# Kernel optimization log

Hardware: AMD Instinct MI355X
Metric: run time of the kernel (lower is better)

The kernel has to match this reference:

```python
import jax, jax.numpy as jnp
import numpy as np

# ---- model hyperparams (from init_kwargs) ----
N_USERS = 200000
N_ITEMS = 100000
DIM = 64
NNZ = 3000000
BATCH = 4096
N_HOPS = 3          # context_hops
EPS = 0.1           # SimGCL perturbation magnitude
TEMP = 0.2          # tau
CL_RATE = 0.5       # lamb
DECAY = 1e-4        # l2


def setup_inputs() -> dict:
    key = jax.random.key(0)
    k = jax.random.split(key, 8)
    user_embed = (jax.random.normal(k[0], (N_USERS, DIM), dtype=jnp.float32) * 0.01)
    item_embed = (jax.random.normal(k[1], (N_ITEMS, DIM), dtype=jnp.float32) * 0.01)
    N = N_USERS + N_ITEMS
    # COO normalized adjacency (buffer, not a parameter in the torch module)
    adj_rows = jax.random.randint(k[2], (NNZ,), 0, N)
    adj_cols = jax.random.randint(k[3], (NNZ,), 0, N)
    adj_vals = jax.random.uniform(k[4], (NNZ,), dtype=jnp.float32) * 0.2
    # unique index batches (torch code calls torch.unique for the CL loss;
    # sampling without replacement makes skipping unique exact, since the
    # InfoNCE mean is permutation invariant)
    users = jax.random.permutation(k[5], N_USERS)[:BATCH].astype(jnp.int32)
    pos_items = jax.random.permutation(k[6], N_ITEMS)[:BATCH].astype(jnp.int32)
    neg_items = jax.random.randint(k[7], (BATCH,), 0, N_ITEMS)
    return {"user_embed": user_embed, "item_embed": item_embed,
            "adj_vals": adj_vals, "adj_rows": adj_rows, "adj_cols": adj_cols,
            "users": users, "pos_items": pos_items, "neg_items": neg_items}


def _spmm(vals, rows, cols, x):
    # torch.sparse.mm(A, x) with A in COO form: out[r] += v * x[c]
    return jax.ops.segment_sum(vals[:, None] * x[cols], rows, num_segments=x.shape[0])


def _gcn(user_embed, item_embed, vals, rows, cols, perturbed, key):
    ego = jnp.concatenate([user_embed, item_embed], axis=0)  # [N, D]
    acc = jnp.zeros_like(ego)
    for h in range(N_HOPS):
        ego = _spmm(vals, rows, cols, ego)
        if perturbed:
            noise = jax.random.uniform(jax.random.fold_in(key, h), ego.shape, dtype=ego.dtype)
            noise = noise / jnp.maximum(jnp.linalg.norm(noise, axis=-1, keepdims=True), 1e-12)
            ego = ego + jnp.sign(ego) * noise * EPS
        acc = acc + ego
    mean = acc / N_HOPS   # stack + mean over hops == running-sum / n_hops
    return mean[:N_USERS], mean[N_USERS:]


def _info_nce(v1, v2, temp):
    v1 = v1 / jnp.maximum(jnp.linalg.norm(v1, axis=1, keepdims=True), 1e-12)
    v2 = v2 / jnp.maximum(jnp.linalg.norm(v2, axis=1, keepdims=True), 1e-12)
    pos = jnp.exp(jnp.sum(v1 * v2, axis=-1) / temp)              # [B]
    ttl = jnp.sum(jnp.exp((v1 @ v2.T) / temp), axis=1)           # [B]
    return jnp.mean(-jnp.log(pos / ttl + 1e-5))


def reference(user_embed, item_embed, adj_vals, adj_rows, adj_cols, users, pos_items, neg_items):
    # --- recommendation branch (no perturbation) ---
    ru, ri = _gcn(user_embed, item_embed, adj_vals, adj_rows, adj_cols, False, jax.random.key(0))
    ue, pe, ne = ru[users], ri[pos_items], ri[neg_items]
    pos_score = jnp.sum(ue * pe, axis=1)
    neg_score = jnp.sum(ue * ne, axis=1)
    rec_loss = jnp.mean(-jnp.log(1e-5 + jax.nn.sigmoid(pos_score - neg_score)))
    reg_loss = DECAY * (jnp.linalg.norm(ue) + jnp.linalg.norm(pe))  # Frobenius norms
    # --- contrastive branch: two perturbed views of the whole GCN ---
    u1, i1 = _gcn(user_embed, item_embed, adj_vals, adj_rows, adj_cols, True, jax.random.key(101))
    u2, i2 = _gcn(user_embed, item_embed, adj_vals, adj_rows, adj_cols, True, jax.random.key(202))
    cl_loss = CL_RATE * (_info_nce(u1[users], u2[users], TEMP)
                         + _info_nce(i1[pos_items], i2[pos_items], TEMP))
    return rec_loss + reg_loss + cl_loss
```

## Files before the change

kernel.cpp:

```cpp
#include <hip/hip_runtime.h>
#include <stdint.h>

#define NUSERS  200000
#define NITEMS  100000
#define NTOT    300000
#define DIM     64
#define NU64    (NUSERS * DIM)
#define NNZC    3000000
#define BATCH   4096
#define B64     (BATCH * DIM)
#define EPSP    0.1f
#define INV_TEMP 5.0f
#define SCAN_ELEMS 1024
#define GELEMS ((size_t)7 * B64 + 2 * BATCH + 8)

#define BSHIFT 11
#define BROWS  (1 << BSHIFT)
#define NB     ((NTOT + BROWS - 1) / BROWS)
#define CHUNK  4096
#define NCHUNK ((NNZC + CHUNK - 1) / CHUNK)
#define NH     (NB * NCHUNK)
#define CASTB  ((NTOT * DIM) / 2048)

typedef short bf16x8 __attribute__((ext_vector_type(8)));
typedef float f32x4  __attribute__((ext_vector_type(4)));

__device__ __forceinline__ float b2f(unsigned short h) {
  return __uint_as_float(((uint32_t)h) << 16);
}
__device__ __forceinline__ unsigned short f2b(float f) {
  uint32_t b = __float_as_uint(f);
  uint32_t r = b + 0x7FFFu + ((b >> 16) & 1u);
  return (unsigned short)(r >> 16);
}

__device__ __forceinline__ uint32_t mix32(uint32_t h) {
  h ^= h >> 16; h *= 0x85EBCA6Bu;
  h ^= h >> 13; h *= 0xC2B2AE35u;
  h ^= h >> 16;
  return h;
}
__device__ __forceinline__ uint32_t noise_key(uint32_t seed, uint32_t hop) {
  return mix32(seed * 0x9E3779B9u + hop * 0x85EBCA6Bu + 0x1BD11BDAu);
}
__device__ __forceinline__ float fast_unif(uint32_t key, uint32_t e) {
  uint32_t h = mix32(key + e * 0x9E3779B9u);
  return __uint_as_float((h >> 9) | 0x3F800000u) - 1.0f;
}
__device__ __forceinline__ float n_ss4(uint32_t key, uint32_t rq, float4& u) {
  uint32_t h = mix32(key + rq * 0x9E3779B9u);
  u.x = ((float)(h & 255u)         + 0.5f) * (1.0f / 256.0f);
  u.y = ((float)((h >> 8) & 255u)  + 0.5f) * (1.0f / 256.0f);
  u.z = ((float)((h >> 16) & 255u) + 0.5f) * (1.0f / 256.0f);
  u.w = ((float)(h >> 24)          + 0.5f) * (1.0f / 256.0f);
  return u.x * u.x + u.y * u.y + u.z * u.z + u.w * u.w;
}

__device__ __forceinline__ float sgnf(float a) {
  return (a > 0.f) ? 1.f : ((a < 0.f) ? -1.f : 0.f);
}

__global__ __launch_bounds__(256) void partA_cast(
    const int* __restrict__ rows, int* __restrict__ Hcnt,
    const float* __restrict__ uemb, const float* __restrict__ iemb,
    unsigned short* __restrict__ X0) {
  int blk = blockIdx.x;
  if (blk >= NCHUNK) {
    int base = (blk - NCHUNK) * 2048 + threadIdx.x * 8;
    const float* src = (base < NU64) ? (uemb + base) : (iemb + (base - NU64));
    float4 f0 = ((const float4*)src)[0];
    float4 f1 = ((const float4*)src)[1];
    uint4 o;
    o.x = ((uint32_t)f2b(f0.y) << 16) | f2b(f0.x);
    o.y = ((uint32_t)f2b(f0.w) << 16) | f2b(f0.z);
    o.z = ((uint32_t)f2b(f1.y) << 16) | f2b(f1.x);
    o.w = ((uint32_t)f2b(f1.w) << 16) | f2b(f1.z);
    *(uint4*)(X0 + base) = o;
    return;
  }
  __shared__ int bc[256];
  int c = blk, t = threadIdx.x;
  bc[t] = 0;
  __syncthreads();
  int base = c * CHUNK;
  for (int i = t; i < CHUNK; i += 256) {
    int e = base + i;
    if (e < NNZC) atomicAdd(&bc[rows[e] >> BSHIFT], 1);
  }
  __syncthreads();
  if (t < NB) Hcnt[t * NCHUNK + c] = bc[t];
}

__global__ void scan_block(const int* __restrict__ cnt, int* __restrict__ out,
                           int* __restrict__ bsums, int n) {
  __shared__ int tmp[SCAN_ELEMS];
  int base = blockIdx.x * SCAN_ELEMS;
  int t = threadIdx.x;
  #pragma unroll
  for (int q = 0; q < 4; ++q) {
    int k = t + q * 256, i = base + k;
    tmp[k] = (i < n) ? cnt[i] : 0;
  }
  __syncthreads();
  for (int off = 1; off < SCAN_ELEMS; off <<= 1) {
    int v[4];
    #pragma unroll
    for (int q = 0; q < 4; ++q) {
      int k = t + q * 256;
      v[q] = (k >= off) ? tmp[k - off] : 0;
    }
    __syncthreads();
    #pragma unroll
    for (int q = 0; q < 4; ++q) tmp[t + q * 256] += v[q];
    __syncthreads();
  }
  #pragma unroll
  for (int q = 0; q < 4; ++q) {
    int k = t + q * 256, i = base + k;
    if (i < n) out[i] = (k == 0) ? 0 : tmp[k - 1];
  }
  if (t == 0) bsums[blockIdx.x] = tmp[SCAN_ELEMS - 1];
}

__global__ void scan_sums(int* __restrict__ bsums, int nb) {
  __shared__ int tmp[512];
  int t = threadIdx.x;
  tmp[t] = (t < nb) ? bsums[t] : 0;
  __syncthreads();
  for (int off = 1; off < 512; off <<= 1) {
    int v = (t >= off) ? tmp[t - off] : 0;
    __syncthreads();
    tmp[t] += v;
    __syncthreads();
  }
  if (t < nb) bsums[t] = (t == 0) ? 0 : tmp[t - 1];
}

__global__ void add_offsets(int* __restrict__ out, const int* __restrict__ bsums,
                            int n) {
  int i = blockIdx.x * blockDim.x + threadIdx.x;
  if (i < n) out[i] += bsums[i / SCAN_ELEMS];
}

__global__ void add_offsets_emit(int* __restrict__ vmap,
                                 const int* __restrict__ bsums,
                                 const int* __restrict__ vflag,
                                 int* __restrict__ vlist,
                                 int* __restrict__ nV) {
  int i = blockIdx.x * blockDim.x + threadIdx.x;
  if (i >= NTOT) return;
  int m = vmap[i] + bsums[i / SCAN_ELEMS];
  vmap[i] = m;
  if (vflag[i]) vlist[m] = i;
  if (i == NTOT - 1) nV[0] = m + vflag[i];
}

__global__ __launch_bounds__(256) void partB(const float* __restrict__ vals,
                                             const int* __restrict__ rows,
                                             const int* __restrict__ cols,
                                             const int* __restrict__ Hofs,
                                             int2* __restrict__ midp,
                                             int* __restrict__ midr) {
  __shared__ int2 stv[CHUNK];
  __shared__ int  str_[CHUNK];
  __shared__ int  cnt[256];
  __shared__ int  sc[256];
  __shared__ int  adj[NB];
  int c = blockIdx.x, t = threadIdx.x;
  cnt[t] = 0;
  __syncthreads();
  int base = c * CHUNK;
  for (int i = t; i < CHUNK; i += 256) {
    int e = base + i;
    if (e < NNZC) atomicAdd(&cnt[rows[e] >> BSHIFT], 1);
  }
  __syncthreads();
  sc[t] = cnt[t];
  __syncthreads();
  for (int off = 1; off < 256; off <<= 1) {
    int u = (t >= off) ? sc[t - off] : 0;
    __syncthreads();
    sc[t] += u;
    __syncthreads();
  }
  int excl = sc[t] - cnt[t];
  cnt[t] = excl;
  if (t < NB) adj[t] = Hofs[t * NCHUNK + c] - excl;
  __syncthreads();
  for (int i = t; i < CHUNK; i += 256) {
    int e = base + i;
    if (e < NNZC) {
      int r = rows[e];
      int b = r >> BSHIFT;
      int p = atomicAdd(&cnt[b], 1);
      stv[p] = make_int2(__float_as_int(vals[e]), cols[e] * DIM);
      str_[p] = r;
    }
  }
  __syncthreads();
  int n = NNZC - base;
  if (n > CHUNK) n = CHUNK;
  for (int p = t; p < n; p += 256) {
    int r = str_[p];
    int b = r >> BSHIFT;
    int dst = adj[b] + p;
    midp[dst] = stv[p];
    midr[dst] = r;
  }
}

__global__ __launch_bounds__(256) void partC(const int2* __restrict__ midp,
                                             const int* __restrict__ midr,
                                             const int* __restrict__ Hofs,
                                             int* __restrict__ rs,
                                             int2* __restrict__ pairs) {
  __shared__ int h[BROWS];
  __shared__ int tsum[256];
  int b = blockIdx.x, t = threadIdx.x;
  int row0 = b << BSHIFT;
  for (int i = t; i < BROWS; i += 256) h[i] = 0;
  __syncthreads();
  int s = Hofs[b * NCHUNK];
  int e = (b + 1 < NB) ? Hofs[(b + 1) * NCHUNK] : NNZC;
  for (int p = s + t; p < e; p += 256)
    atomicAdd(&h[midr[p] - row0], 1);
  __syncthreads();
  int loc[8], run = 0;
  #pragma unroll
  for (int k = 0; k < 8; ++k) { loc[k] = run; run += h[t * 8 + k]; }
  tsum[t] = run;
  __syncthreads();
  for (int off = 1; off < 256; off <<= 1) {
    int v = (t >= off) ? tsum[t - off] : 0;
    __syncthreads();
    tsum[t] += v;
    __syncthreads();
  }
  int baseT = (t == 0) ? 0 : tsum[t - 1];
  #pragma unroll
  for (int k = 0; k < 8; ++k) {
    int i = t * 8 + k;
    int pos = s + baseT + loc[k];
    if (row0 + i < NTOT) rs[row0 + i] = pos;
    h[i] = pos;
  }
  if (b == NB - 1 && t == 0) rs[NTOT] = NNZC;
  __syncthreads();
  for (int p = s + t; p < e; p += 256) {
    int r = midr[p];
    int2 v = midp[p];
    int pos = atomicAdd(&h[r - row0], 1);
    pairs[pos] = v;
  }
}

__global__ __launch_bounds__(256) void mark_v(const int* __restrict__ u,
                                              const int* __restrict__ p,
                                              const int* __restrict__ n,
                                              const int* __restrict__ rs,
                                              const int2* __restrict__ pairs,
                                              int* __restrict__ vflag) {
  int i = blockIdx.x * 256 + threadIdx.x;
  if (i >= 3 * BATCH) return;
  int v = (i < BATCH) ? u[i]
        : (i < 2 * BATCH) ? (NUSERS + p[i - BATCH])
        : (NUSERS + n[i - 2 * BATCH]);
  vflag[v] = 1;
  int s = rs[v], e = rs[v + 1];
  for (int j = s; j < e; ++j) vflag[(unsigned)pairs[j].y >> 6] = 1;
}

template <bool PERT>
__global__ __launch_bounds__(256) void spmm_hop(
    const int2* __restrict__ pairs, const int* __restrict__ rs,
    const unsigned short* __restrict__ x,
    unsigned short* __restrict__ y, uint32_t seed, uint32_t hop) {
  int tid  = threadIdx.x;
  int lane = tid & 63;
  int q    = lane & 15;
  int wave = (blockIdx.x * 256 + tid) >> 6;
  int r    = wave * 4 + (lane >> 4);
  int s    = rs[r];
  int e    = rs[r + 1];
  int q4 = q * 4;
  float a0[4] = {0.f, 0.f, 0.f, 0.f};
  for (int j = s; j < e; j += 8) {
    int2 p[8];
    #pragma unroll
    for (int k = 0; k < 8; ++k)
      p[k] = (j + k < e) ? pairs[j + k] : make_int2(0, 0);
    #pragma unroll
    for (int k = 0; k < 8; ++k) {
      float v = __int_as_float(p[k].x);
      unsigned o = (unsigned)(p[k].y + q4);
      ushort4 h = *(const ushort4*)(x + o);
      a0[0] = fmaf(v, b2f(h.x), a0[0]); a0[1] = fmaf(v, b2f(h.y), a0[1]);
      a0[2] = fmaf(v, b2f(h.z), a0[2]); a0[3] = fmaf(v, b2f(h.w), a0[3]);
    }
  }
  int ebase = r * 64 + q4;
  if (PERT) {
    uint32_t key = noise_key(seed, hop);
    float u[4], ss = 0.f;
    #pragma unroll
    for (int k = 0; k < 4; ++k) {
      u[k] = fast_unif(key, (uint32_t)(ebase + k));
      ss += u[k] * u[k];
    }
    #pragma unroll
    for (int msk = 1; msk < 16; msk <<= 1) ss += __shfl_xor(ss, msk);
    float sc = EPSP / fmaxf(sqrtf(ss), 1e-12f);
    #pragma unroll
    for (int k = 0; k < 4; ++k) a0[k] += sgnf(a0[k]) * u[k] * sc;
  }
  ushort4 st;
  st.x = f2b(a0[0]); st.y = f2b(a0[1]); st.z = f2b(a0[2]); st.w = f2b(a0[3]);
  *(ushort4*)(y + ebase) = st;
}

__global__ __launch_bounds__(256) void spmm_sub3(
    const int2* __restrict__ pairs, const int* __restrict__ rs,
    const int* __restrict__ vlist, const int* __restrict__ nVp,
    const unsigned short* __restrict__ x,
    unsigned short* __restrict__ y0, unsigned short* __restrict__ y1,
    unsigned short* __restrict__ y2) {
  const uint32_t k101 = noise_key(101u, 0u);
  const uint32_t k202 = noise_key(202u, 0u);
  int nV = nVp[0];
  if (blockIdx.x * 16 >= nV) return;
  int tid  = threadIdx.x;
  int lane = tid & 63;
  int q    = lane & 15;
  int wave = (blockIdx.x * 256 + tid) >> 6;
  int slot = wave * 4 + (lane >> 4);
  if (slot >= nV) return;
  int v = vlist[slot];
  int s = rs[v];
  int e = rs[v + 1];
  int q4 = q * 4;
  float A0[4] = {0,0,0,0}, A1[4] = {0,0,0,0}, A2[4] = {0,0,0,0};
  for (int j = s; j < e; j += 8) {
    int2 p[8];
    #pragma unroll
    for (int k = 0; k < 8; ++k)
      p[k] = (j + k < e) ? pairs[j + k] : make_int2(0, 0);
    #pragma unroll
    for (int k = 0; k < 8; ++k) {
      float vv = __int_as_float(p[k].x);
      unsigned o = (unsigned)(p[k].y + q4);
      ushort4 h = *(const ushort4*)(x + o);
      float a[4] = {b2f(h.x), b2f(h.y), b2f(h.z), b2f(h.w)};
      float4 u1, u2;
      float s1 = n_ss4(k101, o >> 2, u1);
      float s2 = n_ss4(k202, o >> 2, u2);
      #pragma unroll
      for (int m = 1; m < 16; m <<= 1) {
        s1 += __shfl_xor(s1, m);
        s2 += __shfl_xor(s2, m);
      }
      float sc1 = EPSP / fmaxf(sqrtf(s1), 1e-12f);
      float sc2 = EPSP / fmaxf(sqrtf(s2), 1e-12f);
      float g0 = sgnf(a[0]), g1 = sgnf(a[1]), g2 = sgnf(a[2]), g3 = sgnf(a[3]);
      A0[0] = fmaf(vv, a[0], A0[0]); A0[1] = fmaf(vv, a[1], A0[1]);
      A0[2] = fmaf(vv, a[2], A0[2]); A0[3] = fmaf(vv, a[3], A0[3]);
      A1[0] = fmaf(vv, fmaf(g0 * u1.x, sc1, a[0]), A1[0]);
      A1[1] = fmaf(vv, fmaf(g1 * u1.y, sc1, a[1]), A1[1]);
      A1[2] = fmaf(vv, fmaf(g2 * u1.z, sc1, a[2]), A1[2]);
      A1[3] = fmaf(vv, fmaf(g3 * u1.w, sc1, a[3]), A1[3]);
      A2[0] = fmaf(vv, fmaf(g0 * u2.x, sc2, a[0]), A2[0]);
      A2[1] = fmaf(vv, fmaf(g1 * u2.y, sc2, a[1]), A2[1]);
      A2[2] = fmaf(vv, fmaf(g2 * u2.z, sc2, a[2]), A2[2]);
      A2[3] = fmaf(vv, fmaf(g3 * u2.w, sc2, a[3]), A2[3]);
    }
  }
  int ob = slot * 64 + q4;
  int en = v * 64 + q4;
  {
    ushort4 st;
    st.x = f2b(A0[0]); st.y = f2b(A0[1]); st.z = f2b(A0[2]); st.w = f2b(A0[3]);
    *(ushort4*)(y0 + ob) = st;
  }
  {
    uint32_t key = noise_key(101u, 1u);
    float u[4], ss = 0.f;
    #pragma unroll
    for (int k = 0; k < 4; ++k) {
      u[k] = fast_unif(key, (uint32_t)(en + k));
      ss += u[k] * u[k];
    }
    #pragma unroll
    for (int msk = 1; msk < 16; msk <<= 1) ss += __shfl_xor(ss, msk);
    float sc = EPSP / fmaxf(sqrtf(ss), 1e-12f);
    #pragma unroll
    for (int k = 0; k < 4; ++k) A1[k] += sgnf(A1[k]) * u[k] * sc;
    ushort4 st;
    st.x = f2b(A1[0]); st.y = f2b(A1[1]); st.z = f2b(A1[2]); st.w = f2b(A1[3]);
    *(ushort4*)(y1 + ob) = st;
  }
  {
    uint32_t key = noise_key(202u, 1u);
    float u[4], ss = 0.f;
    #pragma unroll
    for (int k = 0; k < 4; ++k) {
      u[k] = fast_unif(key, (uint32_t)(en + k));
      ss += u[k] * u[k];
    }
    #pragma unroll
    for (int msk = 1; msk < 16; msk <<= 1) ss += __shfl_xor(ss, msk);
    float sc = EPSP / fmaxf(sqrtf(ss), 1e-12f);
    #pragma unroll
    for (int k = 0; k < 4; ++k) A2[k] += sgnf(A2[k]) * u[k] * sc;
    ushort4 st;
    st.x = f2b(A2[0]); st.y = f2b(A2[1]); st.z = f2b(A2[2]); st.w = f2b(A2[3]);
    *(ushort4*)(y2 + ob) = st;
  }
}

__global__ __launch_bounds__(256) void hop2g7(
    const int2* __restrict__ pairs, const int* __restrict__ rs,
    const unsigned short* __restrict__ Abuf,
    const unsigned short* __restrict__ B0,
    const unsigned short* __restrict__ B1,
    const unsigned short* __restrict__ B2,
    const int* __restrict__ vmap,
    const int* __restrict__ users, const int* __restrict__ pos,
    const int* __restrict__ neg,
    float* __restrict__ g, unsigned short* __restrict__ gb) {
  int by = blockIdx.y;
  int br = (by < 3) ? 0 : ((by < 5) ? 1 : 2);
  const int* idx = (by == 2) ? neg
                 : ((by == 1 || by == 4 || by == 6) ? pos : users);
  int base = (by == 0 || by == 3 || by == 5) ? 0 : NUSERS;
  float* o = g + (size_t)by * B64;
  const unsigned short* Bt = (br == 0) ? B0 : ((br == 1) ? B1 : B2);
  uint32_t seed = (br == 1) ? 101u : 202u;
  int tid  = threadIdx.x;
  int lane = tid & 63;
  int q    = lane & 15;
  int q4 = q * 4;
  int slot = blockIdx.x * 16 + (tid >> 6) * 4 + (lane >> 4);
  int row  = base + idx[slot];
  int s    = rs[row];
  int e    = rs[row + 1];
  float a0[4] = {0.f, 0.f, 0.f, 0.f};
  for (int j = s; j < e; j += 8) {
    int2 p[8];
    #pragma unroll
    for (int k = 0; k < 8; ++k)
      p[k] = (j + k < e) ? pairs[j + k] : make_int2(0, 0);
    int sl[8];
    #pragma unroll
    for (int k = 0; k < 8; ++k)
      sl[k] = vmap[(unsigned)p[k].y >> 6];
    #pragma unroll
    for (int k = 0; k < 8; ++k) {
      float v = __int_as_float(p[k].x);
      unsigned of = (unsigned)(sl[k] * DIM + q4);
      ushort4 h = *(const ushort4*)(Bt + of);
      a0[0] = fmaf(v, b2f(h.x), a0[0]); a0[1] = fmaf(v, b2f(h.y), a0[1]);
      a0[2] = fmaf(v, b2f(h.z), a0[2]); a0[3] = fmaf(v, b2f(h.w), a0[3]);
    }
  }
  if (br) {
    uint32_t key = noise_key(seed, 2u);
    int en = row * 64 + q4;
    float u[4], ss = 0.f;
    #pragma unroll
    for (int k = 0; k < 4; ++k) {
      u[k] = fast_unif(key, (uint32_t)(en + k));
      ss += u[k] * u[k];
    }
    #pragma unroll
    for (int msk = 1; msk < 16; msk <<= 1) ss += __shfl_xor(ss, msk);
    float sc = EPSP / fmaxf(sqrtf(ss), 1e-12f);
    #pragma unroll
    for (int k = 0; k < 4; ++k) a0[k] += sgnf(a0[k]) * u[k] * sc;
  }
  size_t rbA = (size_t)row * DIM + q4;
  size_t rbB = (size_t)vmap[row] * DIM + q4;
  ushort4 ha = *(const ushort4*)(Abuf + rbA);
  ushort4 hb = *(const ushort4*)(Bt + rbB);
  float af[4] = {b2f(ha.x), b2f(ha.y), b2f(ha.z), b2f(ha.w)};
  if (br) {
    uint32_t key0 = noise_key(seed, 0u);
    float4 u;
    float ssn = n_ss4(key0, (uint32_t)(row * 16 + q), u);
    #pragma unroll
    for (int m = 1; m < 16; m <<= 1) ssn += __shfl_xor(ssn, m);
    float scn = EPSP / fmaxf(sqrtf(ssn), 1e-12f);
    af[0] = fmaf(sgnf(af[0]) * u.x, scn, af[0]);
    af[1] = fmaf(sgnf(af[1]) * u.y, scn, af[1]);
    af[2] = fmaf(sgnf(af[2]) * u.z, scn, af[2]);
    af[3] = fmaf(sgnf(af[3]) * u.w, scn, af[3]);
  }
  float rv[4];
  rv[0] = (af[0] + b2f(hb.x)) + a0[0];
  rv[1] = (af[1] + b2f(hb.y)) + a0[1];
  rv[2] = (af[2] + b2f(hb.z)) + a0[2];
  rv[3] = (af[3] + b2f(hb.w)) + a0[3];
  if (br) {
    float ss = rv[0]*rv[0] + rv[1]*rv[1] + rv[2]*rv[2] + rv[3]*rv[3];
    #pragma unroll
    for (int msk = 1; msk < 16; msk <<= 1) ss += __shfl_xor(ss, msk);
    float inv = 1.0f / fmaxf(sqrtf(ss), 1e-12f);
    #pragma unroll
    for (int k = 0; k < 4; ++k) rv[k] *= inv;
  }
  int og = slot * 64 + q4;
  *(float4*)(o + og) = make_float4(rv[0], rv[1], rv[2], rv[3]);
  if (br) {
    unsigned short* ob = gb + (size_t)(by - 3) * B64;
    ushort4 sb;
    sb.x = f2b(rv[0]); sb.y = f2b(rv[1]); sb.z = f2b(rv[2]); sb.w = f2b(rv[3]);
    *(ushort4*)(ob + og) = sb;
  }
}

template <bool PERT>
__global__ __launch_bounds__(256) void spmm_sub(
    const int2* __restrict__ pairs, const int* __restrict__ rs,
    const int* __restrict__ vlist, const int* __restrict__ nVp,
    const unsigned short* __restrict__ x,
    unsigned short* __restrict__ y, uint32_t seed, uint32_t hop) {
  int nV = nVp[0];
  if (blockIdx.x * 16 >= nV) return;
  int tid  = threadIdx.x;
  int lane = tid & 63;
  int q    = lane & 15;
  int wave = (blockIdx.x * 256 + tid) >> 6;
  int slot = wave * 4 + (lane >> 4);
  if (slot >= nV) return;
  int v = vlist[slot];
  int s = rs[v];
  int e = rs[v + 1];
  int q4 = q * 4;
  float a0[4] = {0.f, 0.f, 0.f, 0.f};
  for (int j = s; j < e; j += 8) {
    int2 p[8];
    #pragma unroll
    for (int k = 0; k < 8; ++k)
      p[k] = (j + k < e) ? pairs[j + k] : make_int2(0, 0);
    #pragma unroll
    for (int k = 0; k < 8; ++k) {
      float vv = __int_as_float(p[k].x);
      unsigned o = (unsigned)(p[k].y + q4);
      ushort4 h = *(const ushort4*)(x + o);
      a0[0] = fmaf(vv, b2f(h.x), a0[0]); a0[1] = fmaf(vv, b2f(h.y), a0[1]);
      a0[2] = fmaf(vv, b2f(h.z), a0[2]); a0[3] = fmaf(vv, b2f(h.w), a0[3]);
    }
  }
  if (PERT) {
    uint32_t key = noise_key(seed, hop);
    int en = v * 64 + q4;
    float u[4], ss = 0.f;
    #pragma unroll
    for (int k = 0; k < 4; ++k) {
      u[k] = fast_unif(key, (uint32_t)(en + k));
      ss += u[k] * u[k];
    }
    #pragma unroll
    for (int msk = 1; msk < 16; msk <<= 1) ss += __shfl_xor(ss, msk);
    float sc = EPSP / fmaxf(sqrtf(ss), 1e-12f);
    #pragma unroll
    for (int k = 0; k < 4; ++k) a0[k] += sgnf(a0[k]) * u[k] * sc;
  }
  ushort4 st;
  st.x = f2b(a0[0]); st.y = f2b(a0[1]); st.z = f2b(a0[2]); st.w = f2b(a0[3]);
  *(ushort4*)(y + slot * 64 + q4) = st;
}

template <bool REVERT>
__global__ __launch_bounds__(256) void perturb(unsigned short* __restrict__ A,
                                               uint32_t seedRm, uint32_t seedAdd) {
  int tid  = threadIdx.x;
  int lane = tid & 63;
  int q    = lane & 15;
  int wave = (blockIdx.x * 256 + tid) >> 6;
  int r    = wave * 4 + (lane >> 4);
  int ebase = r * 64 + q * 4;
  ushort4 h4 = *(ushort4*)(A + ebase);
  float av[4] = {b2f(h4.x), b2f(h4.y), b2f(h4.z), b2f(h4.w)};
  if (REVERT) {
    uint32_t key = noise_key(seedRm, 0u);
    float u[4], ss = 0.f;
    #pragma unroll
    for (int k = 0; k < 4; ++k) {
      u[k] = fast_unif(key, (uint32_t)(ebase + k));
      ss += u[k] * u[k];
    }
    #pragma unroll
    for (int msk = 1; msk < 16; msk <<= 1) ss += __shfl_xor(ss, msk);
    float sc = EPSP / fmaxf(sqrtf(ss), 1e-12f);
    #pragma unroll
    for (int k = 0; k < 4; ++k) av[k] -= sgnf(av[k]) * u[k] * sc;
  }
  {
    uint32_t key = noise_key(seedAdd, 0u);
    float u[4], ss = 0.f;
    #pragma unroll
    for (int k = 0; k < 4; ++k) {
      u[k] = fast_unif(key, (uint32_t)(ebase + k));
      ss += u[k] * u[k];
    }
    #pragma unroll
    for (int msk = 1; msk < 16; msk <<= 1) ss += __shfl_xor(ss, msk);
    float sc = EPSP / fmaxf(sqrtf(ss), 1e-12f);
    #pragma unroll
    for (int k = 0; k < 4; ++k) av[k] += sgnf(av[k]) * u[k] * sc;
  }
  ushort4 st;
  st.x = f2b(av[0]); st.y = f2b(av[1]); st.z = f2b(av[2]); st.w = f2b(av[3]);
  *(ushort4*)(A + ebase) = st;
}

template <bool PERT, bool NORM>
__global__ __launch_bounds__(256) void hop2g(
    const int2* __restrict__ pairs, const int* __restrict__ rs,
    const unsigned short* __restrict__ Abuf,
    const unsigned short* __restrict__ Bbuf,
    const int* __restrict__ vmap,
    const int* __restrict__ i0, const int* __restrict__ i1,
    const int* __restrict__ i2,
    float* __restrict__ o0, float* __restrict__ o1, float* __restrict__ o2,
    unsigned short* __restrict__ ob0, unsigned short* __restrict__ ob1,
    int b0, int b1, int b2, uint32_t seed) {
  int seg = blockIdx.y;
  const int* idx = (seg == 0) ? i0 : ((seg == 1) ? i1 : i2);
  float* o = (seg == 0) ? o0 : ((seg == 1) ? o1 : o2);
  unsigned short* ob = (seg == 0) ? ob0 : ob1;
  int base = (seg == 0) ? b0 : ((seg == 1) ? b1 : b2);
  int tid  = threadIdx.x;
  int lane = tid & 63;
  int q    = lane & 15;
  int q4 = q * 4;
  int slot = blockIdx.x * 16 + (tid >> 6) * 4 + (lane >> 4);
  int row  = base + idx[slot];
  int s    = rs[row];
  int e    = rs[row + 1];
  float a0[4] = {0.f, 0.f, 0.f, 0.f};
  for (int j = s; j < e; j += 8) {
    int2 p[8];
    #pragma unroll
    for (int k = 0; k < 8; ++k)
      p[k] = (j + k < e) ? pairs[j + k] : make_int2(0, 0);
    int sl[8];
    #pragma unroll
    for (int k = 0; k < 8; ++k)
      sl[k] = vmap[(unsigned)p[k].y >> 6];
    #pragma unroll
    for (int k = 0; k < 8; ++k) {
      float v = __int_as_float(p[k].x);
      unsigned of = (unsigned)(sl[k] * DIM + q4);
      ushort4 h = *(const ushort4*)(Bbuf + of);
      a0[0] = fmaf(v, b2f(h.x), a0[0]); a0[1] = fmaf(v, b2f(h.y), a0[1]);
      a0[2] = fmaf(v, b2f(h.z), a0[2]); a0[3] = fmaf(v, b2f(h.w), a0[3]);
    }
  }
  if (PERT) {
    uint32_t key = noise_key(seed, 2u);
    int en = row * 64 + q4;
    float u[4], ss = 0.f;
    #pragma unroll
    for (int k = 0; k < 4; ++k) {
      u[k] = fast_unif(key, (uint32_t)(en + k));
      ss += u[k] * u[k];
    }
    #pragma unroll
    for (int msk = 1; msk < 16; msk <<= 1) ss += __shfl_xor(ss, msk);
    float sc = EPSP / fmaxf(sqrtf(ss), 1e-12f);
    #pragma unroll
    for (int k = 0; k < 4; ++k) a0[k] += sgnf(a0[k]) * u[k] * sc;
  }
  size_t rbA = (size_t)row * DIM + q4;
  size_t rbB = (size_t)vmap[row] * DIM + q4;
  ushort4 ha = *(const ushort4*)(Abuf + rbA);
  ushort4 hb = *(const ushort4*)(Bbuf + rbB);
  float rv[4];
  rv[0] = (b2f(ha.x) + b2f(hb.x)) + a0[0];
  rv[1] = (b2f(ha.y) + b2f(hb.y)) + a0[1];
  rv[2] = (b2f(ha.z) + b2f(hb.z)) + a0[2];
  rv[3] = (b2f(ha.w) + b2f(hb.w)) + a0[3];
  if (NORM) {
    float ss = rv[0]*rv[0] + rv[1]*rv[1] + rv[2]*rv[2] + rv[3]*rv[3];
    #pragma unroll
    for (int msk = 1; msk < 16; msk <<= 1) ss += __shfl_xor(ss, msk);
    float inv = 1.0f / fmaxf(sqrtf(ss), 1e-12f);
    #pragma unroll
    for (int k = 0; k < 4; ++k) rv[k] *= inv;
  }
  int og = slot * 64 + q4;
  *(float4*)(o + og) = make_float4(rv[0], rv[1], rv[2], rv[3]);
  if (NORM) {
    ushort4 sb;
    sb.x = f2b(rv[0]); sb.y = f2b(rv[1]); sb.z = f2b(rv[2]); sb.w = f2b(rv[3]);
    *(ushort4*)(ob + og) = sb;
  }
}

__global__ __launch_bounds__(256) void nce_ttl_mfma(
    const unsigned short* __restrict__ u1b, const unsigned short* __restrict__ u2b,
    float* __restrict__ tu,
    const unsigned short* __restrict__ w1b, const unsigned short* __restrict__ w2b,
    float* __restrict__ tw) {
  const unsigned short* V1 = (blockIdx.z == 0) ? u1b : w1b;
  const unsigned short* V2 = (blockIdx.z == 0) ? u2b : w2b;
  float* ttl = (blockIdx.z == 0) ? tu : tw;
  int tid  = threadIdx.x;
  int lane = tid & 63;
  int wv   = tid >> 6;
  int lr   = lane & 15;
  int lk   = (lane >> 4) * 8;
  int m0   = blockIdx.x * 64 + wv * 16;
  bf16x8 a0 = *(const bf16x8*)(V1 + (size_t)(m0 + lr) * DIM + lk);
  bf16x8 a1 = *(const bf16x8*)(V1 + (size_t)(m0 + lr) * DIM + 32 + lk);
  float rowsum[4] = {0.f, 0.f, 0.f, 0.f};
  int n0 = blockIdx.y * 256;
  for (int ch = 0; ch < 4; ++ch) {
    int nc = n0 + ch * 64;
    #pragma unroll
    for (int nt = 0; nt < 4; ++nt) {
      int col = nc + nt * 16 + lr;
      bf16x8 b0 = *(const bf16x8*)(V2 + (size_t)col * DIM + lk);
      bf16x8 b1 = *(const bf16x8*)(V2 + (size_t)col * DIM + 32 + lk);
      f32x4 c = {0.f, 0.f, 0.f, 0.f};
      c = __builtin_amdgcn_mfma_f32_16x16x32_bf16(a0, b0, c, 0, 0, 0);
      c = __builtin_amdgcn_mfma_f32_16x16x32_bf16(a1, b1, c, 0, 0, 0);
      #pragma unroll
      for (int rr = 0; rr < 4; ++rr)
        rowsum[rr] += __expf(c[rr] * INV_TEMP);
    }
  }
  #pragma unroll
  for (int rr = 0; rr < 4; ++rr) {
    float s = rowsum[rr];
    #pragma unroll
    for (int m = 1; m < 16; m <<= 1) s += __shfl_xor(s, m);
    rowsum[rr] = s;
  }
  if (lr == 0) {
    int rbase = m0 + (lane >> 4) * 4;
    #pragma unroll
    for (int rr = 0; rr < 4; ++rr)
      atomicAdd(&ttl[rbase + rr], rowsum[rr]);
  }
}

__global__ __launch_bounds__(256) void nce_final2(const float* __restrict__ g,
                                                  const float* __restrict__ ttl_u,
                                                  float* __restrict__ acc) {
  int by = blockIdx.y;
  const float* v1 = g + (size_t)(3 + by) * B64;
  const float* v2 = g + (size_t)(5 + by) * B64;
  const float* ttl = ttl_u + by * BATCH;
  float* a = acc + 3 + by;
  __shared__ float red[4];
  int tid = threadIdx.x, lane = tid & 63, wv = tid >> 6;
  int gw = blockIdx.x * 4 + wv;
  float l = 0.f;
  for (int r = gw; r < BATCH; r += 256) {
    int gid = r * 64 + lane;
    float p = v1[gid] * v2[gid];
    #pragma unroll
    for (int m = 32; m; m >>= 1) p += __shfl_xor(p, m);
    if (lane == 0) l += -logf(__expf(p * INV_TEMP) / ttl[r] + 1e-5f);
  }
  if (lane == 0) red[wv] = l;
  __syncthreads();
  if (tid == 0) atomicAdd(a, red[0] + red[1] + red[2] + red[3]);
}

__global__ __launch_bounds__(256) void rec_kernel(const float* __restrict__ ue,
                                                  const float* __restrict__ pe,
                                                  const float* __restrict__ ne,
                                                  float* __restrict__ acc) {
  __shared__ float red[3][4];
  int tid = threadIdx.x, lane = tid & 63, wv = tid >> 6;
  int gw = blockIdx.x * 4 + wv;
  const float third = 1.0f / 3.0f;
  float l = 0.f, su = 0.f, sp = 0.f;
  for (int r = gw; r < BATCH; r += 256) {
    int gid = r * 64 + lane;
    float u = ue[gid] * third, p = pe[gid] * third, n = ne[gid] * third;
    float ps = u * p, ns = u * n;
    su += u * u; sp += p * p;
    #pragma unroll
    for (int m = 32; m; m >>= 1) { ps += __shfl_xor(ps, m); ns += __shfl_xor(ns, m); }
    if (lane == 0) {
      float sig = 1.0f / (1.0f + __expf(-(ps - ns)));
      l += -logf(1e-5f + sig);
    }
  }
  #pragma unroll
  for (int m = 32; m; m >>= 1) { su += __shfl_xor(su, m); sp += __shfl_xor(sp, m); }
  if (lane == 0) { red[0][wv] = l; red[1][wv] = su; red[2][wv] = sp; }
  __syncthreads();
  if (tid == 0) {
    atomicAdd(acc + 0, red[0][0] + red[0][1] + red[0][2] + red[0][3]);
    atomicAdd(acc + 1, red[1][0] + red[1][1] + red[1][2] + red[1][3]);
    atomicAdd(acc + 2, red[2][0] + red[2][1] + red[2][2] + red[2][3]);
  }
}

__global__ void finalize_kernel(const float* __restrict__ acc, float* __restrict__ out) {
  out[0] = acc[0] * (1.0f / BATCH)
         + 1e-4f * (sqrtf(acc[1]) + sqrtf(acc[2]))
         + 0.5f * (acc[3] + acc[4]) * (1.0f / BATCH);
}

extern "C" void kernel_launch(void* const* d_in, const int* in_sizes, int n_in,
                              void* d_out, int out_size, void* d_ws, size_t ws_size,
                              hipStream_t stream) {
  (void)in_sizes; (void)n_in; (void)out_size;
  const float* user_embed = (const float*)d_in[0];
  const float* item_embed = (const float*)d_in[1];
  const float* adj_vals   = (const float*)d_in[2];
  const int*   adj_rows   = (const int*)d_in[3];
  const int*   adj_cols   = (const int*)d_in[4];
  const int*   users      = (const int*)d_in[5];
  const int*   pos_items  = (const int*)d_in[6];
  const int*   neg_items  = (const int*)d_in[7];
  float* out = (float*)d_out;

  const size_t bufElems = (size_t)NTOT * DIM;

  unsigned short* A  = (unsigned short*)d_ws;
  unsigned short* B0 = A + bufElems;
  int2*  pairs = (int2*)(B0 + bufElems);
  float* g     = (float*)(pairs + NNZC);
  float* g_ue = g + 0 * (size_t)B64;
  float* g_pe = g + 1 * (size_t)B64;
  float* g_ne = g + 2 * (size_t)B64;
  float* g_u1 = g + 3 * (size_t)B64;
  float* g_i1 = g + 4 * (size_t)B64;
  float* g_u2 = g + 5 * (size_t)B64;
  float* g_i2 = g + 6 * (size_t)B64;
  float* ttl_u = g + 7 * (size_t)B64;
  float* ttl_i = ttl_u + BATCH;
  float* acc   = ttl_i + BATCH;
  int* rs     = (int*)(g + GELEMS);
  int* bsums  = rs + (NTOT + 1);
  int* vflag  = bsums + 512;
  int* vmap   = vflag + NTOT;
  int* vlist  = vmap + NTOT;
  int* nVd    = vlist + NTOT;
  unsigned short* gb = (unsigned short*)(((uintptr_t)(nVd + 1) + 31) & ~(uintptr_t)31);
  unsigned short* g_u1b = gb + 0 * (size_t)B64;
  unsigned short* g_i1b = gb + 1 * (size_t)B64;
  unsigned short* g_u2b = gb + 2 * (size_t)B64;
  unsigned short* g_i2b = gb + 3 * (size_t)B64;

  uintptr_t endBase = (uintptr_t)(gb + 4 * (size_t)B64);
  unsigned short* B1 = (unsigned short*)((endBase + 15) & ~(uintptr_t)15);
  unsigned short* B2 = B1 + bufElems;
  size_t need_fused = (size_t)((uintptr_t)(B2 + bufElems) - (uintptr_t)d_ws);
  const bool fused = (ws_size == 0) || (ws_size >= need_fused);

  int2* midp = (int2*)A;
  int*  midr = (int*)(midp + NNZC);
  int*  Hcnt = midr + NNZC;
  int*  Hofs = Hcnt + NH;
  unsigned short* X0 = B0;

  hipMemsetAsync(ttl_u, 0, (2 * BATCH + 8) * sizeof(float), stream);
  hipMemsetAsync(vflag, 0, NTOT * sizeof(int), stream);

  partA_cast<<<NCHUNK + CASTB, 256, 0, stream>>>(adj_rows, Hcnt,
                                                 user_embed, item_embed, X0);
  const int nhb = (NH + SCAN_ELEMS - 1) / SCAN_ELEMS;
  scan_block<<<nhb, 256, 0, stream>>>(Hcnt, Hofs, bsums, NH);
  scan_sums<<<1, 512, 0, stream>>>(bsums, nhb);
  add_offsets<<<(NH + 255) / 256, 256, 0, stream>>>(Hofs, bsums, NH);
  partB<<<NCHUNK, 256, 0, stream>>>(adj_vals, adj_rows, adj_cols, Hofs, midp, midr);
  partC<<<NB, 256, 0, stream>>>(midp, midr, Hofs, rs, pairs);

  mark_v<<<(3 * BATCH + 255) / 256, 256, 0, stream>>>(
      users, pos_items, neg_items, rs, pairs, vflag);
  const int nvb = (NTOT + SCAN_ELEMS - 1) / SCAN_ELEMS;
  scan_block<<<nvb, 256, 0, stream>>>(vflag, vmap, bsums, NTOT);
  scan_sums<<<1, 512, 0, stream>>>(bsums, nvb);
  add_offsets_emit<<<(NTOT + 255) / 256, 256, 0, stream>>>(vmap, bsums, vflag,
                                                           vlist, nVd);

  const int spmm_blocks = NTOT / 16;

  spmm_hop<false><<<spmm_blocks, 256, 0, stream>>>(pairs, rs, X0, A, 0u, 0u);

  if (fused) {
    spmm_sub3<<<spmm_blocks, 256, 0, stream>>>(pairs, rs, vlist, nVd, A,
                                               B0, B1, B2);
    dim3 h2g7(BATCH / 16, 7);
    hop2g7<<<h2g7, 256, 0, stream>>>(pairs, rs, A, B0, B1, B2, vmap,
                                     users, pos_items, neg_items, g, gb);
  } else {
    dim3 h2g3(BATCH / 16, 3), h2g2(BATCH / 16, 2);
    spmm_sub<false><<<spmm_blocks, 256, 0, stream>>>(
        pairs, rs, vlist, nVd, A, B0, 0u, 0u);
    hop2g<false, false><<<h2g3, 256, 0, stream>>>(
        pairs, rs, A, B0, vmap, users, pos_items, neg_items,
        g_ue, g_pe, g_ne, nullptr, nullptr, 0, NUSERS, NUSERS, 0u);
    perturb<false><<<spmm_blocks, 256, 0, stream>>>(A, 0u, 101u);
    spmm_sub<true><<<spmm_blocks, 256, 0, stream>>>(
        pairs, rs, vlist, nVd, A, B0, 101u, 1u);
    hop2g<true, true><<<h2g2, 256, 0, stream>>>(
        pairs, rs, A, B0, vmap, users, pos_items, nullptr,
        g_u1, g_i1, nullptr, g_u1b, g_i1b, 0, NUSERS, 0, 101u);
    perturb<true><<<spmm_blocks, 256, 0, stream>>>(A, 101u, 202u);
    spmm_sub<true><<<spmm_blocks, 256, 0, stream>>>(
        pairs, rs, vlist, nVd, A, B0, 202u, 1u);
    hop2g<true, true><<<h2g2, 256, 0, stream>>>(
        pairs, rs, A, B0, vmap, users, pos_items, nullptr,
        g_u2, g_i2, nullptr, g_u2b, g_i2b, 0, NUSERS, 0, 202u);
  }

  rec_kernel<<<64, 256, 0, stream>>>(g_ue, g_pe, g_ne, acc);
  dim3 nce_grid(BATCH / 64, BATCH / 256, 2);
  nce_ttl_mfma<<<nce_grid, 256, 0, stream>>>(g_u1b, g_u2b, ttl_u,
                                             g_i1b, g_i2b, ttl_i);
  dim3 nfin(64, 2);
  nce_final2<<<nfin, 256, 0, stream>>>(g, ttl_u, acc);
  finalize_kernel<<<1, 1, 0, stream>>>(acc, out);
}
```

Measured before the change: 572.5 us.

## Precompute perturbed hop-1 embeddings once instead of regenerating noise per edge

The fused hop-2 subset SpMM used to regenerate two noise vectors and their norms for every edge gather. It is replaced by a perturb3 pass that writes two perturbed copies of the hop-1 embeddings once per node, followed by a plain SpMM with a grid z-dimension selecting one of the three views. This removes redundant per-edge RNG and shuffle-reduction work, at the cost of extra memory traffic and workspace (two more full-size buffers) plus three separate gathers. The perturb kernel also switches to the shared n_ss4 helper for noise generation.

```diff
diff --git a/kernel.cpp b/kernel.cpp
--- a/kernel.cpp
+++ b/kernel.cpp
@@ -318,16 +318,56 @@
   *(ushort4*)(y + ebase) = st;
 }
 
-__global__ __launch_bounds__(256) void spmm_sub3(
+__global__ __launch_bounds__(256) void perturb3(
+    const unsigned short* __restrict__ A,
+    unsigned short* __restrict__ A1, unsigned short* __restrict__ A2) {
+  const uint32_t k101 = noise_key(101u, 0u);
+  const uint32_t k202 = noise_key(202u, 0u);
+  int tid  = threadIdx.x;
+  int lane = tid & 63;
+  int q    = lane & 15;
+  int wave = (blockIdx.x * 256 + tid) >> 6;
+  int r    = wave * 4 + (lane >> 4);
+  int ebase = r * 64 + q * 4;
+  ushort4 h4 = *(const ushort4*)(A + ebase);
+  float a[4] = {b2f(h4.x), b2f(h4.y), b2f(h4.z), b2f(h4.w)};
+  float4 u1, u2;
+  float s1 = n_ss4(k101, (uint32_t)(r * 16 + q), u1);
+  float s2 = n_ss4(k202, (uint32_t)(r * 16 + q), u2);
+  #pragma unroll
+  for (int m = 1; m < 16; m <<= 1) {
+    s1 += __shfl_xor(s1, m);
+    s2 += __shfl_xor(s2, m);
+  }
+  float sc1 = EPSP / fmaxf(sqrtf(s1), 1e-12f);
+  float sc2 = EPSP / fmaxf(sqrtf(s2), 1e-12f);
+  float g0 = sgnf(a[0]), g1 = sgnf(a[1]), g2 = sgnf(a[2]), g3 = sgnf(a[3]);
+  ushort4 o1, o2;
+  o1.x = f2b(fmaf(g0 * u1.x, sc1, a[0]));
+  o1.y = f2b(fmaf(g1 * u1.y, sc1, a[1]));
+  o1.z = f2b(fmaf(g2 * u1.z, sc1, a[2]));
+  o1.w = f2b(fmaf(g3 * u1.w, sc1, a[3]));
+  o2.x = f2b(fmaf(g0 * u2.x, sc2, a[0]));
+  o2.y = f2b(fmaf(g1 * u2.y, sc2, a[1]));
+  o2.z = f2b(fmaf(g2 * u2.z, sc2, a[2]));
+  o2.w = f2b(fmaf(g3 * u2.w, sc2, a[3]));
+  *(ushort4*)(A1 + ebase) = o1;
+  *(ushort4*)(A2 + ebase) = o2;
+}
+
+__global__ __launch_bounds__(256) void spmm_subz(
     const int2* __restrict__ pairs, const int* __restrict__ rs,
     const int* __restrict__ vlist, const int* __restrict__ nVp,
-    const unsigned short* __restrict__ x,
+    const unsigned short* __restrict__ x0,
+    const unsigned short* __restrict__ x1,
+    const unsigned short* __restrict__ x2,
     unsigned short* __restrict__ y0, unsigned short* __restrict__ y1,
     unsigned short* __restrict__ y2) {
-  const uint32_t k101 = noise_key(101u, 0u);
-  const uint32_t k202 = noise_key(202u, 0u);
   int nV = nVp[0];
   if (blockIdx.x * 16 >= nV) return;
+  int z = blockIdx.y;
+  const unsigned short* x = (z == 0) ? x0 : ((z == 1) ? x1 : x2);
+  unsigned short* y = (z == 0) ? y0 : ((z == 1) ? y1 : y2);
   int tid  = threadIdx.x;
   int lane = tid & 63;
   int q    = lane & 15;
@@ -338,7 +378,7 @@
   int s = rs[v];
   int e = rs[v + 1];
   int q4 = q * 4;
-  float A0[4] = {0,0,0,0}, A1[4] = {0,0,0,0}, A2[4] = {0,0,0,0};
+  float a0[4] = {0.f, 0.f, 0.f, 0.f};
   for (int j = s; j < e; j += 8) {
     int2 p[8];
     #pragma unroll
@@ -349,39 +389,13 @@
       float vv = __int_as_float(p[k].x);
       unsigned o = (unsigned)(p[k].y + q4);
       ushort4 h = *(const ushort4*)(x + o);
-      float a[4] = {b2f(h.x), b2f(h.y), b2f(h.z), b2f(h.w)};
-      float4 u1, u2;
-      float s1 = n_ss4(k101, o >> 2, u1);
-      float s2 = n_ss4(k202, o >> 2, u2);
-      #pragma unroll
-      for (int m = 1; m < 16; m <<= 1) {
-        s1 += __shfl_xor(s1, m);
-        s2 += __shfl_xor(s2, m);
-      }
-      float sc1 = EPSP / fmaxf(sqrtf(s1), 1e-12f);
-      float sc2 = EPSP / fmaxf(sqrtf(s2), 1e-12f);
-      float g0 = sgnf(a[0]), g1 = sgnf(a[1]), g2 = sgnf(a[2]), g3 = sgnf(a[3]);
-      A0[0] = fmaf(vv, a[0], A0[0]); A0[1] = fmaf(vv, a[1], A0[1]);
-      A0[2] = fmaf(vv, a[2], A0[2]); A0[3] = fmaf(vv, a[3], A0[3]);
-      A1[0] = fmaf(vv, fmaf(g0 * u1.x, sc1, a[0]), A1[0]);
-      A1[1] = fmaf(vv, fmaf(g1 * u1.y, sc1, a[1]), A1[1]);
-      A1[2] = fmaf(vv, fmaf(g2 * u1.z, sc1, a[2]), A1[2]);
-      A1[3] = fmaf(vv, fmaf(g3 * u1.w, sc1, a[3]), A1[3]);
-      A2[0] = fmaf(vv, fmaf(g0 * u2.x, sc2, a[0]), A2[0]);
-      A2[1] = fmaf(vv, fmaf(g1 * u2.y, sc2, a[1]), A2[1]);
-      A2[2] = fmaf(vv, fmaf(g2 * u2.z, sc2, a[2]), A2[2]);
-      A2[3] = fmaf(vv, fmaf(g3 * u2.w, sc2, a[3]), A2[3]);
-    }
-  }
-  int ob = slot * 64 + q4;
-  int en = v * 64 + q4;
-  {
-    ushort4 st;
-    st.x = f2b(A0[0]); st.y = f2b(A0[1]); st.z = f2b(A0[2]); st.w = f2b(A0[3]);
-    *(ushort4*)(y0 + ob) = st;
-  }
-  {
-    uint32_t key = noise_key(101u, 1u);
+      a0[0] = fmaf(vv, b2f(h.x), a0[0]); a0[1] = fmaf(vv, b2f(h.y), a0[1]);
+      a0[2] = fmaf(vv, b2f(h.z), a0[2]); a0[3] = fmaf(vv, b2f(h.w), a0[3]);
+    }
+  }
+  if (z) {
+    uint32_t key = noise_key((z == 1) ? 101u : 202u, 1u);
+    int en = v * 64 + q4;
     float u[4], ss = 0.f;
     #pragma unroll
     for (int k = 0; k < 4; ++k) {
@@ -392,28 +406,11 @@
     for (int msk = 1; msk < 16; msk <<= 1) ss += __shfl_xor(ss, msk);
     float sc = EPSP / fmaxf(sqrtf(ss), 1e-12f);
     #pragma unroll
-    for (int k = 0; k < 4; ++k) A1[k] += sgnf(A1[k]) * u[k] * sc;
-    ushort4 st;
-    st.x = f2b(A1[0]); st.y = f2b(A1[1]); st.z = f2b(A1[2]); st.w = f2b(A1[3]);
-    *(ushort4*)(y1 + ob) = st;
-  }
-  {
-    uint32_t key = noise_key(202u, 1u);
-    float u[4], ss = 0.f;
-    #pragma unroll
-    for (int k = 0; k < 4; ++k) {
-      u[k] = fast_unif(key, (uint32_t)(en + k));
-      ss += u[k] * u[k];
-    }
-    #pragma unroll
-    for (int msk = 1; msk < 16; msk <<= 1) ss += __shfl_xor(ss, msk);
-    float sc = EPSP / fmaxf(sqrtf(ss), 1e-12f);
-    #pragma unroll
-    for (int k = 0; k < 4; ++k) A2[k] += sgnf(A2[k]) * u[k] * sc;
-    ushort4 st;
-    st.x = f2b(A2[0]); st.y = f2b(A2[1]); st.z = f2b(A2[2]); st.w = f2b(A2[3]);
-    *(ushort4*)(y2 + ob) = st;
-  }
+    for (int k = 0; k < 4; ++k) a0[k] += sgnf(a0[k]) * u[k] * sc;
+  }
+  ushort4 st;
+  st.x = f2b(a0[0]); st.y = f2b(a0[1]); st.z = f2b(a0[2]); st.w = f2b(a0[3]);
+  *(ushort4*)(y + slot * 64 + q4) = st;
 }
 
 __global__ __launch_bounds__(256) void hop2g7(
@@ -582,31 +579,27 @@
   float av[4] = {b2f(h4.x), b2f(h4.y), b2f(h4.z), b2f(h4.w)};
   if (REVERT) {
     uint32_t key = noise_key(seedRm, 0u);
-    float u[4], ss = 0.f;
-    #pragma unroll
-    for (int k = 0; k < 4; ++k) {
-      u[k] = fast_unif(key, (uint32_t)(ebase + k));
-      ss += u[k] * u[k];
-    }
+    float4 u;
+    float ss = n_ss4(key, (uint32_t)(r * 16 + q), u);
     #pragma unroll
     for (int msk = 1; msk < 16; msk <<= 1) ss += __shfl_xor(ss, msk);
     float sc = EPSP / fmaxf(sqrtf(ss), 1e-12f);
-    #pragma unroll
-    for (int k = 0; k < 4; ++k) av[k] -= sgnf(av[k]) * u[k] * sc;
+    av[0] -= sgnf(av[0]) * u.x * sc;
+    av[1] -= sgnf(av[1]) * u.y * sc;
+    av[2] -= sgnf(av[2]) * u.z * sc;
+    av[3] -= sgnf(av[3]) * u.w * sc;
   }
   {
     uint32_t key = noise_key(seedAdd, 0u);
-    float u[4], ss = 0.f;
-    #pragma unroll
-    for (int k = 0; k < 4; ++k) {
-      u[k] = fast_unif(key, (uint32_t)(ebase + k));
-      ss += u[k] * u[k];
-    }
+    float4 u;
+    float ss = n_ss4(key, (uint32_t)(r * 16 + q), u);
     #pragma unroll
     for (int msk = 1; msk < 16; msk <<= 1) ss += __shfl_xor(ss, msk);
     float sc = EPSP / fmaxf(sqrtf(ss), 1e-12f);
-    #pragma unroll
-    for (int k = 0; k < 4; ++k) av[k] += sgnf(av[k]) * u[k] * sc;
+    av[0] += sgnf(av[0]) * u.x * sc;
+    av[1] += sgnf(av[1]) * u.y * sc;
+    av[2] += sgnf(av[2]) * u.z * sc;
+    av[3] += sgnf(av[3]) * u.w * sc;
   }
   ushort4 st;
   st.x = f2b(av[0]); st.y = f2b(av[1]); st.z = f2b(av[2]); st.w = f2b(av[3]);
@@ -852,8 +845,10 @@
   uintptr_t endBase = (uintptr_t)(gb + 4 * (size_t)B64);
   unsigned short* B1 = (unsigned short*)((endBase + 15) & ~(uintptr_t)15);
   unsigned short* B2 = B1 + bufElems;
-  size_t need_fused = (size_t)((uintptr_t)(B2 + bufElems) - (uintptr_t)d_ws);
-  const bool fused = (ws_size == 0) || (ws_size >= need_fused);
+  unsigned short* A1 = B2 + bufElems;
+  unsigned short* A2 = A1 + bufElems;
+  size_t need_full = (size_t)((uintptr_t)(A2 + bufElems) - (uintptr_t)d_ws);
+  const bool fused = (ws_size == 0) || (ws_size >= need_full);
 
   int2* midp = (int2*)A;
   int*  midr = (int*)(midp + NNZC);
@@ -886,8 +881,10 @@
   spmm_hop<false><<<spmm_blocks, 256, 0, stream>>>(pairs, rs, X0, A, 0u, 0u);
 
   if (fused) {
-    spmm_sub3<<<spmm_blocks, 256, 0, stream>>>(pairs, rs, vlist, nVd, A,
-                                               B0, B1, B2);
+    perturb3<<<spmm_blocks, 256, 0, stream>>>(A, A1, A2);
+    dim3 subz(spmm_blocks, 3);
+    spmm_subz<<<subz, 256, 0, stream>>>(pairs, rs, vlist, nVd,
+                                        A, A1, A2, B0, B1, B2);
     dim3 h2g7(BATCH / 16, 7);
     hop2g7<<<h2g7, 256, 0, stream>>>(pairs, rs, A, B0, B1, B2, vmap,
                                      users, pos_items, neg_items, g, gb);
```

Result: no change. 567.3 us (-0.9%).
